# Performance work log

Hardware: AMD Instinct MI355X
Metric: run time of the kernel (lower is better)

Reference implementation:

```python
import jax, jax.numpy as jnp
import numpy as np

SH_C0 = 0.28209479177387814
SH_C1 = 0.4886025119029199
EPS2D = 0.3  # gsplat 'classic' rasterize_mode adds 0.3 to 2D covariance diagonal
NEAR_PLANE = 0.01
FAR_PLANE = 1e10
ALPHA_MIN = 1.0 / 255.0
ALPHA_MAX = 0.999
T_EPS = 1e-4  # gsplat terminates compositing when transmittance drops below this

N_GAUSS = 2048
WIDTH = 160
HEIGHT = 160


def _quat_to_rotmat(q):
    q = q / jnp.linalg.norm(q, axis=-1, keepdims=True)
    w, x, y, z = q[:, 0], q[:, 1], q[:, 2], q[:, 3]
    return jnp.stack([
        1 - 2 * (y * y + z * z), 2 * (x * y - w * z), 2 * (x * z + w * y),
        2 * (x * y + w * z), 1 - 2 * (x * x + z * z), 2 * (y * z - w * x),
        2 * (x * z - w * y), 2 * (y * z + w * x), 1 - 2 * (x * x + y * y),
    ], axis=-1).reshape(-1, 3, 3)


def _forward(means3d, opacities, scales, quats, sh0, shN, camtoworlds, Ks, width, height):
    viewmat = jnp.linalg.inv(camtoworlds)[0]  # world->cam, single camera
    K = Ks[0]
    fx, fy, cx, cy = K[0, 0], K[1, 1], K[0, 2], K[1, 2]
    opac = jax.nn.sigmoid(opacities)
    sh = jnp.concatenate([sh0, shN], axis=1)  # [N,4,3]

    # degree-1 SH -> view-dependent RGB
    campos = camtoworlds[0, :3, 3]
    d = means3d - campos
    d = d / jnp.linalg.norm(d, axis=-1, keepdims=True)
    dxv, dyv, dzv = d[:, 0:1], d[:, 1:2], d[:, 2:3]
    colors = SH_C0 * sh[:, 0] + SH_C1 * (-dyv * sh[:, 1] + dzv * sh[:, 2] - dxv * sh[:, 3]) + 0.5
    colors = jnp.maximum(colors, 0.0)  # [N,3]

    # 3D covariance = R S S^T R^T
    R = _quat_to_rotmat(quats)
    M = R * scales[:, None, :]
    cov3d = M @ jnp.swapaxes(M, 1, 2)  # [N,3,3]

    # project to camera
    W3, t3 = viewmat[:3, :3], viewmat[:3, 3]
    tcam = means3d @ W3.T + t3  # [N,3]
    tz = tcam[:, 2]
    rz = 1.0 / tz
    lim_x = 1.3 * (0.5 * width / fx)
    lim_y = 1.3 * (0.5 * height / fy)
    txz = jnp.clip(tcam[:, 0] * rz, -lim_x, lim_x)
    tyz = jnp.clip(tcam[:, 1] * rz, -lim_y, lim_y)
    zero = jnp.zeros_like(rz)
    J = jnp.stack([
        jnp.stack([fx * rz, zero, -fx * txz * rz], axis=-1),
        jnp.stack([zero, fy * rz, -fy * tyz * rz], axis=-1),
    ], axis=-2)  # [N,2,3]
    cov_cam = jnp.einsum('ij,njk,lk->nil', W3, cov3d, W3)
    cov2d = jnp.einsum('nij,njk,nlk->nil', J, cov_cam, J)  # [N,2,2]
    a = cov2d[:, 0, 0] + EPS2D
    bb = cov2d[:, 0, 1]
    c = cov2d[:, 1, 1] + EPS2D
    det = a * c - bb * bb
    det_safe = jnp.where(det > 0, det, 1.0)
    cA, cB, cC = c / det_safe, -bb / det_safe, a / det_safe  # conic
    mx = fx * tcam[:, 0] * rz + cx
    my = fy * tcam[:, 1] * rz + cy
    valid = (tz > NEAR_PLANE) & (tz < FAR_PLANE) & (det > 0)

    # global front-to-back depth sort (single camera)
    order = jnp.argsort(tz)
    mx, my = mx[order], my[order]
    cA, cB, cC = cA[order], cB[order], cC[order]
    opac_s, colors_s = opac[order], colors[order]
    tz_s, valid_s = tz[order], valid[order]

    # pixel centers, flattened row-major [P = H*W]
    xs = jnp.arange(width, dtype=means3d.dtype) + 0.5
    ys = jnp.arange(height, dtype=means3d.dtype) + 0.5
    px = jnp.tile(xs, height)
    py = jnp.repeat(ys, width)

    dx = px[:, None] - mx[None, :]  # [P,N]
    dy = py[:, None] - my[None, :]
    sigma = 0.5 * (cA[None, :] * dx * dx + cC[None, :] * dy * dy) + cB[None, :] * dx * dy
    alpha = jnp.minimum(ALPHA_MAX, opac_s[None, :] * jnp.exp(-sigma))
    keep = valid_s[None, :] & (sigma >= 0) & (alpha >= ALPHA_MIN)
    alpha = jnp.where(keep, alpha, 0.0)

    T = jnp.cumprod(1.0 - alpha, axis=-1)
    T_excl = jnp.concatenate([jnp.ones_like(T[:, :1]), T[:, :-1]], axis=-1)
    w = jnp.where(T_excl > T_EPS, alpha * T_excl, 0.0)  # [P,N]

    rgb = w @ colors_s                     # [P,3]
    depth = w @ tz_s                       # [P] accumulated depth
    alpha_tot = jnp.sum(w, axis=-1)        # [P]
    ed = depth / jnp.maximum(alpha_tot, 1e-10)  # expected depth ('ED')
    render_colors = jnp.concatenate([rgb, ed[:, None]], axis=-1).reshape(1, height, width, 4)
    render_alphas = alpha_tot.reshape(1, height, width, 1)
    return render_colors, render_alphas


def setup_inputs() -> dict:
    key = jax.random.key(0)
    ks = jax.random.split(key, 6)
    means3d = jax.random.normal(ks[0], (N_GAUSS, 3), jnp.float32) * 1.0 + jnp.array([0.0, 0.0, 4.0])
    opacities = jax.random.normal(ks[1], (N_GAUSS,), jnp.float32)
    scales = jax.random.uniform(ks[2], (N_GAUSS, 3), jnp.float32) * 0.05 + 0.01
    quats = jax.random.normal(ks[3], (N_GAUSS, 4), jnp.float32)
    sh0 = jax.random.normal(ks[4], (N_GAUSS, 1, 3), jnp.float32) * 0.5
    shN = jax.random.normal(ks[5], (N_GAUSS, 3, 3), jnp.float32) * 0.1
    camtoworlds = jnp.eye(4, dtype=jnp.float32)[None]  # camera at origin looking +z
    Ks = jnp.array([[[200.0, 0.0, WIDTH / 2.0], [0.0, 200.0, HEIGHT / 2.0], [0.0, 0.0, 1.0]]], jnp.float32)
    return {"means3d": means3d, "opacities": opacities, "scales": scales, "quats": quats,
            "sh0": sh0, "shN": shN, "camtoworlds": camtoworlds, "Ks": Ks,
            "width": WIDTH, "height": HEIGHT}


def reference(means3d, opacities, scales, quats, sh0, shN, camtoworlds, Ks, width, height):
    return _forward(means3d, opacities, scales, quats, sh0, shN, camtoworlds, Ks, width, height)
```

## Files before the change

### kernel.cpp

```cpp
#include <hip/hip_runtime.h>
#include <math.h>

#define SH_C0f 0.28209479177387814f
#define SH_C1f 0.4886025119029199f
#define EPS2D 0.3f
#define NEAR_PLANE 0.01f
#define FAR_PLANE 1e10f
#define ALPHA_MIN (1.0f/255.0f)
#define ALPHA_MAX 0.999f
#define T_EPS 1e-4f
#define TS 8
#define NW 8

__global__ void preprocess_kernel(
    const float* __restrict__ means, const float* __restrict__ opac_in,
    const float* __restrict__ scales, const float* __restrict__ quats,
    const float* __restrict__ sh0, const float* __restrict__ shN,
    const float* __restrict__ c2w, const float* __restrict__ Ks,
    const int* __restrict__ wptr, const int* __restrict__ hptr,
    float4* __restrict__ attrs, float* __restrict__ tz_arr, int N)
{
    int i = blockIdx.x * blockDim.x + threadIdx.x;
    if (i >= N) return;

    float m[16];
    #pragma unroll
    for (int k = 0; k < 16; k++) m[k] = c2w[k];
    float inv[12];
    inv[0]  =  m[5]*m[10]*m[15] - m[5]*m[11]*m[14] - m[9]*m[6]*m[15] + m[9]*m[7]*m[14] + m[13]*m[6]*m[11] - m[13]*m[7]*m[10];
    inv[4]  = -m[4]*m[10]*m[15] + m[4]*m[11]*m[14] + m[8]*m[6]*m[15] - m[8]*m[7]*m[14] - m[12]*m[6]*m[11] + m[12]*m[7]*m[10];
    inv[8]  =  m[4]*m[9]*m[15]  - m[4]*m[11]*m[13] - m[8]*m[5]*m[15] + m[8]*m[7]*m[13] + m[12]*m[5]*m[11] - m[12]*m[7]*m[9];
    inv[1]  = -m[1]*m[10]*m[15] + m[1]*m[11]*m[14] + m[9]*m[2]*m[15] - m[9]*m[3]*m[14] - m[13]*m[2]*m[11] + m[13]*m[3]*m[10];
    inv[5]  =  m[0]*m[10]*m[15] - m[0]*m[11]*m[14] - m[8]*m[2]*m[15] + m[8]*m[3]*m[14] + m[12]*m[2]*m[11] - m[12]*m[3]*m[10];
    inv[9]  = -m[0]*m[9]*m[15]  + m[0]*m[11]*m[13] + m[8]*m[1]*m[15] - m[8]*m[3]*m[13] - m[12]*m[1]*m[11] + m[12]*m[3]*m[9];
    inv[2]  =  m[1]*m[6]*m[15]  - m[1]*m[7]*m[14]  - m[5]*m[2]*m[15] + m[5]*m[3]*m[14] + m[13]*m[2]*m[7]  - m[13]*m[3]*m[6];
    inv[6]  = -m[0]*m[6]*m[15]  + m[0]*m[7]*m[14]  + m[4]*m[2]*m[15] - m[4]*m[3]*m[14] - m[12]*m[2]*m[7]  + m[12]*m[3]*m[6];
    inv[10] =  m[0]*m[5]*m[15]  - m[0]*m[7]*m[13]  - m[4]*m[1]*m[15] + m[4]*m[3]*m[13] + m[12]*m[1]*m[7]  - m[12]*m[3]*m[5];
    inv[3]  = -m[1]*m[6]*m[11]  + m[1]*m[7]*m[10]  + m[5]*m[2]*m[11] - m[5]*m[3]*m[10] - m[9]*m[2]*m[7]   + m[9]*m[3]*m[6];
    inv[7]  =  m[0]*m[6]*m[11]  - m[0]*m[7]*m[10]  - m[4]*m[2]*m[11] + m[4]*m[3]*m[10] + m[8]*m[2]*m[7]   - m[8]*m[3]*m[6];
    inv[11] = -m[0]*m[5]*m[11]  + m[0]*m[7]*m[9]   + m[4]*m[1]*m[11] - m[4]*m[3]*m[9]  - m[8]*m[1]*m[7]   + m[8]*m[3]*m[5];
    {
        float inv12 = -m[4]*m[9]*m[14] + m[4]*m[10]*m[13] + m[8]*m[5]*m[14] - m[8]*m[6]*m[13] - m[12]*m[5]*m[10] + m[12]*m[6]*m[9];
        float det = m[0]*inv[0] + m[1]*inv[4] + m[2]*inv[8] + m[3]*inv12;
        float r = 1.0f / det;
        #pragma unroll
        for (int k = 0; k < 12; k++) inv[k] *= r;
    }
    const float W00 = inv[0], W01 = inv[1], W02 = inv[2],  t0 = inv[3];
    const float W10 = inv[4], W11 = inv[5], W12 = inv[6],  t1 = inv[7];
    const float W20 = inv[8], W21 = inv[9], W22 = inv[10], t2 = inv[11];

    const float fx = Ks[0], cx = Ks[2], fy = Ks[4], cy = Ks[5];
    const float width = (float)wptr[0], height = (float)hptr[0];

    const float mxx = means[i*3+0], myy = means[i*3+1], mzz = means[i*3+2];

    const float cpx = m[3], cpy = m[7], cpz = m[11];
    float dx = mxx - cpx, dy = myy - cpy, dz = mzz - cpz;
    float dn = sqrtf(dx*dx + dy*dy + dz*dz);
    dx /= dn; dy /= dn; dz /= dn;

    float col[3];
    #pragma unroll
    for (int c = 0; c < 3; c++) {
        float v = SH_C0f * sh0[i*3+c]
                + SH_C1f * (-dy * shN[i*9 + 0*3 + c] + dz * shN[i*9 + 1*3 + c] - dx * shN[i*9 + 2*3 + c])
                + 0.5f;
        col[c] = fmaxf(v, 0.0f);
    }

    const float op = 1.0f / (1.0f + expf(-opac_in[i]));

    float qw = quats[i*4+0], qx = quats[i*4+1], qy = quats[i*4+2], qz = quats[i*4+3];
    float qn = sqrtf(qw*qw + qx*qx + qy*qy + qz*qz);
    qw /= qn; qx /= qn; qy /= qn; qz /= qn;
    const float R00 = 1.f - 2.f*(qy*qy + qz*qz), R01 = 2.f*(qx*qy - qw*qz), R02 = 2.f*(qx*qz + qw*qy);
    const float R10 = 2.f*(qx*qy + qw*qz), R11 = 1.f - 2.f*(qx*qx + qz*qz), R12 = 2.f*(qy*qz - qw*qx);
    const float R20 = 2.f*(qx*qz - qw*qy), R21 = 2.f*(qy*qz + qw*qx), R22 = 1.f - 2.f*(qx*qx + qy*qy);

    const float sx = scales[i*3+0], sy = scales[i*3+1], sz = scales[i*3+2];
    const float M00 = R00*sx, M01 = R01*sy, M02 = R02*sz;
    const float M10 = R10*sx, M11 = R11*sy, M12 = R12*sz;
    const float M20 = R20*sx, M21 = R21*sy, M22 = R22*sz;

    const float S00 = M00*M00 + M01*M01 + M02*M02;
    const float S01 = M00*M10 + M01*M11 + M02*M12;
    const float S02 = M00*M20 + M01*M21 + M02*M22;
    const float S11 = M10*M10 + M11*M11 + M12*M12;
    const float S12 = M10*M20 + M11*M21 + M12*M22;
    const float S22 = M20*M20 + M21*M21 + M22*M22;

    const float tcx = W00*mxx + W01*myy + W02*mzz + t0;
    const float tcy = W10*mxx + W11*myy + W12*mzz + t1;
    const float tcz = W20*mxx + W21*myy + W22*mzz + t2;
    const float rz = 1.0f / tcz;

    const float limx = 1.3f * (0.5f * width / fx);
    const float limy = 1.3f * (0.5f * height / fy);
    const float txz = fminf(fmaxf(tcx * rz, -limx), limx);
    const float tyz = fminf(fmaxf(tcy * rz, -limy), limy);

    const float V00 = W00*S00 + W01*S01 + W02*S02;
    const float V01 = W00*S01 + W01*S11 + W02*S12;
    const float V02 = W00*S02 + W01*S12 + W02*S22;
    const float V10 = W10*S00 + W11*S01 + W12*S02;
    const float V11 = W10*S01 + W11*S11 + W12*S12;
    const float V12 = W10*S02 + W11*S12 + W12*S22;
    const float V20 = W20*S00 + W21*S01 + W22*S02;
    const float V21 = W20*S01 + W21*S11 + W22*S12;
    const float V22 = W20*S02 + W21*S12 + W22*S22;
    const float CC00 = V00*W00 + V01*W01 + V02*W02;
    const float CC01 = V00*W10 + V01*W11 + V02*W12;
    const float CC02 = V00*W20 + V01*W21 + V02*W22;
    const float CC11 = V10*W10 + V11*W11 + V12*W12;
    const float CC12 = V10*W20 + V11*W21 + V12*W22;
    const float CC22 = V20*W20 + V21*W21 + V22*W22;

    const float j00 = fx * rz,  j02 = -fx * txz * rz;
    const float j11 = fy * rz,  j12 = -fy * tyz * rz;

    const float u0 = j00*CC00 + j02*CC02;
    const float u1 = j00*CC01 + j02*CC12;
    const float u2 = j00*CC02 + j02*CC22;
    const float v1 = j11*CC11 + j12*CC12;
    const float v2 = j11*CC12 + j12*CC22;
    const float c2d00 = u0*j00 + u2*j02;
    const float c2d01 = u1*j11 + u2*j12;
    const float c2d11 = v1*j11 + v2*j12;

    const float a  = c2d00 + EPS2D;
    const float bb = c2d01;
    const float cc = c2d11 + EPS2D;
    const float det = a*cc - bb*bb;
    const float det_safe = (det > 0.0f) ? det : 1.0f;
    const float invd = 1.0f / det_safe;

    const bool valid = (tcz > NEAR_PLANE) && (tcz < FAR_PLANE) && (det > 0.0f);

    float rad = 0.0f;
    if (valid && op >= ALPHA_MIN) {
        const float lmax = 0.5f*(a + cc) + sqrtf(fmaxf(0.f, 0.25f*(a - cc)*(a - cc) + bb*bb));
        const float sig_cut = logf(255.0f * op);
        rad = sqrtf(fmaxf(sig_cut, 0.0f) * 2.0f * lmax) * 1.001f + 0.5f;
    }

    const float mx2d = fx * tcx * rz + cx;
    const float my2d = fy * tcy * rz + cy;

    attrs[i*3+0] = make_float4(mx2d, my2d, 0.5f * cc * invd, -bb * invd);
    attrs[i*3+1] = make_float4(0.5f * a * invd, op, tcz, rad);
    attrs[i*3+2] = make_float4(col[0], col[1], col[2], 0.0f);
    tz_arr[i] = tcz;
}

__global__ __launch_bounds__(64) void sort_scatter_kernel(
    const float* __restrict__ tz, const float4* __restrict__ attrs,
    float4* __restrict__ attrs_s, float4* __restrict__ bounds_s, int N)
{
    const int i = blockIdx.x;
    const int lane = threadIdx.x;
    const float k = tz[i];

    int rank = 0;
    int j = lane * 4;
    const int Nv = N & ~3;
    for (; j + 3 < Nv; j += 256) {
        const float4 v = *reinterpret_cast<const float4*>(tz + j);
        rank += (v.x < k) || (v.x == k && (j + 0) < i);
        rank += (v.y < k) || (v.y == k && (j + 1) < i);
        rank += (v.z < k) || (v.z == k && (j + 2) < i);
        rank += (v.w < k) || (v.w == k && (j + 3) < i);
    }
    const int t = Nv + lane;
    if (t < N) {
        const float kj = tz[t];
        rank += (kj < k) || (kj == k && t < i);
    }

    #pragma unroll
    for (int off = 32; off > 0; off >>= 1) rank += __shfl_down(rank, off);
    rank = __shfl(rank, 0);

    if (lane < 3) attrs_s[rank*3 + lane] = attrs[i*3 + lane];
    if (lane == 3) {
        const float4 g0 = attrs[i*3+0];
        const float4 g1 = attrs[i*3+1];
        bounds_s[rank] = make_float4(g0.x, g0.y, g1.w, 0.0f);
    }
}

__device__ __forceinline__ float eval_alpha(const float4 g0, const float4 g1,
                                            const float px, const float py) {
    const float ddx = px - g0.x;
    const float ddy = py - g0.y;
    const float sg = g0.z*ddx*ddx + g1.x*ddy*ddy + g0.w*ddx*ddy;
    float a = g1.y * expf(-sg);
    return ((sg >= 0.0f) && (a >= ALPHA_MIN)) ? fminf(a, ALPHA_MAX) : 0.0f;
}

__global__ __launch_bounds__(512) void raster_kernel(
    const float4* __restrict__ attrs_s, const float4* __restrict__ bounds_s,
    float* __restrict__ out, int N, int P, const int* __restrict__ wptr)
{
    extern __shared__ int smem[];
    __shared__ float s_P[NW][64];
    __shared__ float s_red[NW][64][5];

    const int width  = wptr[0];
    const int height = P / width;
    const int tilesX = (width  + TS - 1) / TS;
    const int tilesY = (height + TS - 1) / TS;
    const int nTiles = tilesX * tilesY;
    const int lane = threadIdx.x & 63;
    const int wv   = threadIdx.x >> 6;

    const int NR = (((N + NW - 1) / NW) + 63) & ~63;
    int* s_list = smem + wv * NR;
    const int rstart = wv * NR;
    const int rend   = min(rstart + NR, N);

    for (int tile = blockIdx.x; tile < nTiles; tile += gridDim.x) {
        __syncthreads();

        const int tx = tile % tilesX, ty = tile / tilesX;
        const float x0 = (float)(tx*TS) + 0.5f;
        const float x1 = (float)(min(tx*TS + TS - 1, width  - 1)) + 0.5f;
        const float y0 = (float)(ty*TS) + 0.5f;
        const float y1 = (float)(min(ty*TS + TS - 1, height - 1)) + 0.5f;

        int count = 0;
        for (int base = rstart; base < rend; base += 64) {
            const int j = base + lane;
            bool pred = false;
            if (j < rend) {
                const float4 b = bounds_s[j];
                pred = (b.z > 0.0f) &&
                       (b.x + b.z >= x0) && (b.x - b.z <= x1) &&
                       (b.y + b.z >= y0) && (b.y - b.z <= y1);
            }
            const unsigned long long m = __ballot(pred);
            const int pre = __popcll(m & ((1ull << lane) - 1ull));
            if (pred) s_list[count + pre] = j;
            count += (int)__popcll(m);
        }
        __syncthreads();

        const int px_i = tx*TS + (lane & (TS-1));
        const int py_i = ty*TS + (lane >> 3);
        const bool active = (px_i < width) && (py_i < height);
        const float px = (float)px_i + 0.5f;
        const float py = (float)py_i + 0.5f;

        float Tl = 1.0f;
        float accr = 0.f, accg = 0.f, accb = 0.f, accd = 0.f, acca = 0.f;
        for (int p = 0; p < count; p += 4) {
            const int4 s4 = *reinterpret_cast<const int4*>(&s_list[p]);
            int id[4];
            id[0] = s4.x;
            id[1] = (p+1 < count) ? s4.y : s4.x;
            id[2] = (p+2 < count) ? s4.z : s4.x;
            id[3] = (p+3 < count) ? s4.w : s4.x;
            float al[4];
            float4 G1[4], G2[4];
            #pragma unroll
            for (int u = 0; u < 4; u++) {
                const int idx = __builtin_amdgcn_readfirstlane(id[u]);
                const float4 g0 = attrs_s[idx*3+0];
                G1[u] = attrs_s[idx*3+1];
                G2[u] = attrs_s[idx*3+2];
                const float a = eval_alpha(g0, G1[u], px, py);
                al[u] = (p+u < count) ? a : 0.0f;
            }
            #pragma unroll
            for (int u = 0; u < 4; u++) {
                const float w = al[u] * Tl;
                accr += w * G2[u].x;
                accg += w * G2[u].y;
                accb += w * G2[u].z;
                accd += w * G1[u].z;
                acca += w;
                Tl *= (1.0f - al[u]);
            }
            if (__all(Tl <= T_EPS)) break;
        }
        s_P[wv][lane] = Tl;
        __syncthreads();

        float Ts = active ? 1.0f : 0.0f;
        for (int m = 0; m < wv; m++) Ts *= s_P[m][lane];

        s_red[wv][lane][0] = accr * Ts;
        s_red[wv][lane][1] = accg * Ts;
        s_red[wv][lane][2] = accb * Ts;
        s_red[wv][lane][3] = accd * Ts;
        s_red[wv][lane][4] = acca * Ts;
        __syncthreads();

        if (wv == 0 && active) {
            float r = 0.f, g = 0.f, b = 0.f, d = 0.f, a = 0.f;
            #pragma unroll
            for (int m = 0; m < NW; m++) {
                r += s_red[m][lane][0];
                g += s_red[m][lane][1];
                b += s_red[m][lane][2];
                d += s_red[m][lane][3];
                a += s_red[m][lane][4];
            }
            const int pix = py_i * width + px_i;
            out[pix*4 + 0] = r;
            out[pix*4 + 1] = g;
            out[pix*4 + 2] = b;
            out[pix*4 + 3] = d / fmaxf(a, 1e-10f);
            out[(size_t)P*4 + pix] = a;
        }
    }
}

extern "C" void kernel_launch(void* const* d_in, const int* in_sizes, int n_in,
                              void* d_out, int out_size, void* d_ws, size_t ws_size,
                              hipStream_t stream) {
    const float* means   = (const float*)d_in[0];
    const float* opac    = (const float*)d_in[1];
    const float* scales  = (const float*)d_in[2];
    const float* quats   = (const float*)d_in[3];
    const float* sh0     = (const float*)d_in[4];
    const float* shN     = (const float*)d_in[5];
    const float* c2w     = (const float*)d_in[6];
    const float* Ks      = (const float*)d_in[7];
    const int*   wptr    = (const int*)d_in[8];
    const int*   hptr    = (const int*)d_in[9];

    const int N = in_sizes[0] / 3;
    const int P = out_size / 5;

    float4* attrs    = (float4*)d_ws;
    float4* attrs_s  = attrs + 3*N;
    float4* bounds_s = attrs_s + 3*N;
    float*  tz_u     = (float*)(bounds_s + N);

    const int gb = (N + 255) / 256;
    hipLaunchKernelGGL(preprocess_kernel, dim3(gb), dim3(256), 0, stream,
                       means, opac, scales, quats, sh0, shN, c2w, Ks, wptr, hptr,
                       attrs, tz_u, N);

    hipLaunchKernelGGL(sort_scatter_kernel, dim3(N), dim3(64), 0, stream,
                       tz_u, attrs, attrs_s, bounds_s, N);

    const int NR = (((N + NW - 1) / NW) + 63) & ~63;
    const size_t lds = (size_t)NW * NR * sizeof(int);
    hipLaunchKernelGGL(raster_kernel, dim3(512), dim3(512), lds, stream,
                       attrs_s, bounds_s, (float*)d_out, N, P, wptr);
}
```

Before: 21.58 us.

## Replace global depth sort kernel with per-tile LDS rank sort in raster

Removes the separate global rank-sort-and-scatter kernel and instead has each raster tile block cull gaussians in unsorted order, then rank-sort only its own culled list by depth in shared memory. The culled list is now built block-wide with a per-wave count exchange, and each wave composites a contiguous segment of the sorted list. This eliminates one kernel launch and the N-block global sort in exchange for an O(count^2) per-tile sort and extra syncthreads in the culling loop. Attribute loads now gather from the unsorted array.

```diff
diff --git a/kernel.cpp b/kernel.cpp
--- a/kernel.cpp
+++ b/kernel.cpp
@@ -18,7 +18,7 @@
     const float* __restrict__ sh0, const float* __restrict__ shN,
     const float* __restrict__ c2w, const float* __restrict__ Ks,
     const int* __restrict__ wptr, const int* __restrict__ hptr,
-    float4* __restrict__ attrs, float* __restrict__ tz_arr, int N)
+    float4* __restrict__ attrs, float4* __restrict__ bounds, int N)
 {
     int i = blockIdx.x * blockDim.x + threadIdx.x;
     if (i >= N) return;
@@ -150,43 +150,7 @@
     attrs[i*3+0] = make_float4(mx2d, my2d, 0.5f * cc * invd, -bb * invd);
     attrs[i*3+1] = make_float4(0.5f * a * invd, op, tcz, rad);
     attrs[i*3+2] = make_float4(col[0], col[1], col[2], 0.0f);
-    tz_arr[i] = tcz;
-}
-
-__global__ __launch_bounds__(64) void sort_scatter_kernel(
-    const float* __restrict__ tz, const float4* __restrict__ attrs,
-    float4* __restrict__ attrs_s, float4* __restrict__ bounds_s, int N)
-{
-    const int i = blockIdx.x;
-    const int lane = threadIdx.x;
-    const float k = tz[i];
-
-    int rank = 0;
-    int j = lane * 4;
-    const int Nv = N & ~3;
-    for (; j + 3 < Nv; j += 256) {
-        const float4 v = *reinterpret_cast<const float4*>(tz + j);
-        rank += (v.x < k) || (v.x == k && (j + 0) < i);
-        rank += (v.y < k) || (v.y == k && (j + 1) < i);
-        rank += (v.z < k) || (v.z == k && (j + 2) < i);
-        rank += (v.w < k) || (v.w == k && (j + 3) < i);
-    }
-    const int t = Nv + lane;
-    if (t < N) {
-        const float kj = tz[t];
-        rank += (kj < k) || (kj == k && t < i);
-    }
-
-    #pragma unroll
-    for (int off = 32; off > 0; off >>= 1) rank += __shfl_down(rank, off);
-    rank = __shfl(rank, 0);
-
-    if (lane < 3) attrs_s[rank*3 + lane] = attrs[i*3 + lane];
-    if (lane == 3) {
-        const float4 g0 = attrs[i*3+0];
-        const float4 g1 = attrs[i*3+1];
-        bounds_s[rank] = make_float4(g0.x, g0.y, g1.w, 0.0f);
-    }
+    bounds[i]   = make_float4(mx2d, my2d, rad, 0.0f);
 }
 
 __device__ __forceinline__ float eval_alpha(const float4 g0, const float4 g1,
@@ -199,10 +163,14 @@
 }
 
 __global__ __launch_bounds__(512) void raster_kernel(
-    const float4* __restrict__ attrs_s, const float4* __restrict__ bounds_s,
+    const float4* __restrict__ attrs, const float4* __restrict__ bounds,
     float* __restrict__ out, int N, int P, const int* __restrict__ wptr)
 {
     extern __shared__ int smem[];
+    int*   s_list   = smem;
+    float* s_keys   = (float*)(smem + N);
+    int*   s_sorted = smem + 2*N;
+    __shared__ int   s_wcnt[NW];
     __shared__ float s_P[NW][64];
     __shared__ float s_red[NW][64][5];
 
@@ -211,13 +179,9 @@
     const int tilesX = (width  + TS - 1) / TS;
     const int tilesY = (height + TS - 1) / TS;
     const int nTiles = tilesX * tilesY;
-    const int lane = threadIdx.x & 63;
-    const int wv   = threadIdx.x >> 6;
-
-    const int NR = (((N + NW - 1) / NW) + 63) & ~63;
-    int* s_list = smem + wv * NR;
-    const int rstart = wv * NR;
-    const int rend   = min(rstart + NR, N);
+    const int tid  = threadIdx.x;
+    const int lane = tid & 63;
+    const int wv   = tid >> 6;
 
     for (int tile = blockIdx.x; tile < nTiles; tile += gridDim.x) {
         __syncthreads();
@@ -229,19 +193,42 @@
         const float y1 = (float)(min(ty*TS + TS - 1, height - 1)) + 0.5f;
 
         int count = 0;
-        for (int base = rstart; base < rend; base += 64) {
-            const int j = base + lane;
+        for (int base = 0; base < N; base += 512) {
+            const int j = base + tid;
             bool pred = false;
-            if (j < rend) {
-                const float4 b = bounds_s[j];
+            if (j < N) {
+                const float4 b = bounds[j];
                 pred = (b.z > 0.0f) &&
                        (b.x + b.z >= x0) && (b.x - b.z <= x1) &&
                        (b.y + b.z >= y0) && (b.y - b.z <= y1);
             }
             const unsigned long long m = __ballot(pred);
             const int pre = __popcll(m & ((1ull << lane) - 1ull));
-            if (pred) s_list[count + pre] = j;
-            count += (int)__popcll(m);
+            if (lane == 0) s_wcnt[wv] = (int)__popcll(m);
+            __syncthreads();
+            int off = count + pre;
+            int tot = 0;
+            #pragma unroll
+            for (int w = 0; w < NW; w++) {
+                if (w < wv) off += s_wcnt[w];
+                tot += s_wcnt[w];
+            }
+            if (pred) s_list[off] = j;
+            count += tot;
+            __syncthreads();
+        }
+
+        for (int t = tid; t < count; t += 512)
+            s_keys[t] = attrs[s_list[t]*3 + 1].z;
+        __syncthreads();
+        for (int t = tid; t < count; t += 512) {
+            const float kt = s_keys[t];
+            int rank = 0;
+            for (int mIdx = 0; mIdx < count; mIdx++) {
+                const float km = s_keys[mIdx];
+                rank += (km < kt) || (km == kt && mIdx < t);
+            }
+            s_sorted[rank] = s_list[t];
         }
         __syncthreads();
 
@@ -251,25 +238,27 @@
         const float px = (float)px_i + 0.5f;
         const float py = (float)py_i + 0.5f;
 
+        const int seg    = (count + NW - 1) / NW;
+        const int cstart = wv * seg;
+        const int cend   = min(cstart + seg, count);
+
         float Tl = 1.0f;
         float accr = 0.f, accg = 0.f, accb = 0.f, accd = 0.f, acca = 0.f;
-        for (int p = 0; p < count; p += 4) {
-            const int4 s4 = *reinterpret_cast<const int4*>(&s_list[p]);
+        for (int p = cstart; p < cend; p += 4) {
             int id[4];
-            id[0] = s4.x;
-            id[1] = (p+1 < count) ? s4.y : s4.x;
-            id[2] = (p+2 < count) ? s4.z : s4.x;
-            id[3] = (p+3 < count) ? s4.w : s4.x;
             float al[4];
             float4 G1[4], G2[4];
             #pragma unroll
+            for (int u = 0; u < 4; u++)
+                id[u] = s_sorted[(p+u < cend) ? (p+u) : p];
+            #pragma unroll
             for (int u = 0; u < 4; u++) {
                 const int idx = __builtin_amdgcn_readfirstlane(id[u]);
-                const float4 g0 = attrs_s[idx*3+0];
-                G1[u] = attrs_s[idx*3+1];
-                G2[u] = attrs_s[idx*3+2];
+                const float4 g0 = attrs[idx*3+0];
+                G1[u] = attrs[idx*3+1];
+                G2[u] = attrs[idx*3+2];
                 const float a = eval_alpha(g0, G1[u], px, py);
-                al[u] = (p+u < count) ? a : 0.0f;
+                al[u] = (p+u < cend) ? a : 0.0f;
             }
             #pragma unroll
             for (int u = 0; u < 4; u++) {
@@ -333,21 +322,15 @@
     const int N = in_sizes[0] / 3;
     const int P = out_size / 5;
 
-    float4* attrs    = (float4*)d_ws;
-    float4* attrs_s  = attrs + 3*N;
-    float4* bounds_s = attrs_s + 3*N;
-    float*  tz_u     = (float*)(bounds_s + N);
+    float4* attrs  = (float4*)d_ws;
+    float4* bounds = attrs + 3*N;
 
     const int gb = (N + 255) / 256;
     hipLaunchKernelGGL(preprocess_kernel, dim3(gb), dim3(256), 0, stream,
                        means, opac, scales, quats, sh0, shN, c2w, Ks, wptr, hptr,
-                       attrs, tz_u, N);
-
-    hipLaunchKernelGGL(sort_scatter_kernel, dim3(N), dim3(64), 0, stream,
-                       tz_u, attrs, attrs_s, bounds_s, N);
-
-    const int NR = (((N + NW - 1) / NW) + 63) & ~63;
-    const size_t lds = (size_t)NW * NR * sizeof(int);
+                       attrs, bounds, N);
+
+    const size_t lds = (size_t)3 * N * sizeof(int);
     hipLaunchKernelGGL(raster_kernel, dim3(512), dim3(512), lds, stream,
-                       attrs_s, bounds_s, (float*)d_out, N, P, wptr);
+                       attrs, bounds, (float*)d_out, N, P, wptr);
 }
```

Measured after the change: 20.63 us. 4.4% less time.
